# Kernel optimization log

Measured on AMD Instinct MI355X. Metric: run time of the kernel, lower is better.

Reference implementation:

```python
import jax, jax.numpy as jnp
import numpy as np

N = 100000      # nodes
E = 1600000     # edges
G = 1024        # graphs in batch
NF = 9          # atom features (OGB AtomEncoder)
V = 128         # vocab per atom feature
H = 128         # hidden_dim
L = 3           # num_graph_layers
OUT = 10        # output_dim
BN_EPS = 1e-5


def setup_inputs() -> dict:
    key = jax.random.key(0)
    ks = jax.random.split(key, 12)
    x = jax.random.randint(ks[0], (N, NF), 0, V, dtype=jnp.int32)
    edge_index = jax.random.randint(ks[1], (2, E), 0, N, dtype=jnp.int32)
    batch = jnp.sort(jax.random.randint(ks[2], (N,), 0, G, dtype=jnp.int32))
    emb = jax.random.normal(ks[3], (NF, V, H), dtype=jnp.float32) * 0.05
    Ws = jax.random.normal(ks[4], (L, H, H), dtype=jnp.float32) * (1.0 / np.sqrt(H))
    bs = jnp.zeros((L, H), dtype=jnp.float32)
    gamma = jnp.ones((L - 1, H), dtype=jnp.float32)
    beta = jnp.zeros((L - 1, H), dtype=jnp.float32)
    run_mean = jax.random.normal(ks[5], (L - 1, H), dtype=jnp.float32) * 0.1
    run_var = jax.random.uniform(ks[6], (L - 1, H), minval=0.5, maxval=1.5, dtype=jnp.float32)
    W_clf = jax.random.normal(ks[7], (H, OUT), dtype=jnp.float32) * (1.0 / np.sqrt(H))
    b_clf = jnp.zeros((OUT,), dtype=jnp.float32)
    return {"x": x, "edge_index": edge_index, "batch": batch, "emb": emb,
            "Ws": Ws, "bs": bs, "gamma": gamma, "beta": beta,
            "run_mean": run_mean, "run_var": run_var,
            "W_clf": W_clf, "b_clf": b_clf}


def reference(x, edge_index, batch, emb, Ws, bs, gamma, beta, run_mean, run_var, W_clf, b_clf):
    # Eval-mode forward: dropout = identity, BatchNorm uses running stats.
    src, dst = edge_index[0], edge_index[1]
    # GCN symmetric normalization with self-loops: deg = 1 + in-degree
    deg = jax.ops.segment_sum(jnp.ones((E,), jnp.float32), dst, num_segments=N) + 1.0
    dinv = jax.lax.rsqrt(deg)                 # [N]
    norm_e = dinv[src] * dinv[dst]            # [E] edge coefficient
    norm_self = dinv * dinv                   # [N] self-loop coefficient

    # AtomEncoder: sum of per-feature embedding lookups -> [N, H]
    h = emb[jnp.arange(NF)[None, :], x].sum(axis=1)

    for i in range(L):
        hw = h @ Ws[i]                                                       # [N, H]
        h = (jax.ops.segment_sum(hw[src] * norm_e[:, None], dst, num_segments=N)
             + hw * norm_self[:, None] + bs[i])                              # GCNConv
        if i < L - 1:
            h = (h - run_mean[i]) * (gamma[i] * jax.lax.rsqrt(run_var[i] + BN_EPS)) + beta[i]
            h = jax.nn.relu(h)

    # global mean pool over graphs
    counts = jax.ops.segment_sum(jnp.ones((N,), jnp.float32), batch, num_segments=G)
    pooled = jax.ops.segment_sum(h, batch, num_segments=G) / jnp.maximum(counts, 1.0)[:, None]
    return pooled @ W_clf + b_clf             # [G, OUT]
```

## Files before the change

### kernel.cpp

```cpp
#include <hip/hip_runtime.h>
#include <hip/hip_bf16.h>
#include <hip/hip_fp16.h>

#define NN 100000
#define EE 1600000
#define GG 1024
#define NF 9
#define VV 128
#define HH 128
#define LL 3
#define OUTD 10
#define BN_EPS 1e-5f
#define NB_SCAN 98
#define NBUCK 196
#define BCAP 12288
#define CHUNK 4096
#define NB64 1563

typedef __attribute__((ext_vector_type(8))) short short8;
typedef __attribute__((ext_vector_type(8))) _Float16 half8;
typedef __attribute__((ext_vector_type(4))) float f32x4;

__device__ inline unsigned short f2bf(float x) {
    unsigned u = __float_as_uint(x);
    unsigned r = (u + 0x7fffu + ((u >> 16) & 1u)) >> 16;
    return (unsigned short)r;
}
__device__ inline float bf2f(unsigned short b) { return __uint_as_float(((unsigned)b) << 16); }

__device__ inline void mix8(float a[8], const uint4& r, float nm) {
    asm("v_fma_mix_f32 %0, %8, %12, %0 op_sel:[0,0,0] op_sel_hi:[1,0,0]\n\t"
        "v_fma_mix_f32 %1, %8, %12, %1 op_sel:[1,0,0] op_sel_hi:[1,0,0]\n\t"
        "v_fma_mix_f32 %2, %9, %12, %2 op_sel:[0,0,0] op_sel_hi:[1,0,0]\n\t"
        "v_fma_mix_f32 %3, %9, %12, %3 op_sel:[1,0,0] op_sel_hi:[1,0,0]\n\t"
        "v_fma_mix_f32 %4, %10, %12, %4 op_sel:[0,0,0] op_sel_hi:[1,0,0]\n\t"
        "v_fma_mix_f32 %5, %10, %12, %5 op_sel:[1,0,0] op_sel_hi:[1,0,0]\n\t"
        "v_fma_mix_f32 %6, %11, %12, %6 op_sel:[0,0,0] op_sel_hi:[1,0,0]\n\t"
        "v_fma_mix_f32 %7, %11, %12, %7 op_sel:[1,0,0] op_sel_hi:[1,0,0]"
        : "+v"(a[0]), "+v"(a[1]), "+v"(a[2]), "+v"(a[3]),
          "+v"(a[4]), "+v"(a[5]), "+v"(a[6]), "+v"(a[7])
        : "v"(r.x), "v"(r.y), "v"(r.z), "v"(r.w), "v"(nm));
}

__device__ inline void fma4(float4& a, const float4 r, float nm) {
    a.x = fmaf(r.x, nm, a.x); a.y = fmaf(r.y, nm, a.y);
    a.z = fmaf(r.z, nm, a.z); a.w = fmaf(r.w, nm, a.w);
}

__global__ __launch_bounds__(256) void split_kernel(const int* __restrict__ src,
                                                    const int* __restrict__ dst,
                                                    int* __restrict__ bcur,
                                                    int* __restrict__ bucket_edges) {
    __shared__ int lcnt[256], loff[256], lcur[256], gbase[256], sh[256];
    __shared__ int stage[CHUNK];
    __shared__ unsigned char stageb[CHUNK];
    int tid = threadIdx.x;
    int cs = blockIdx.x * CHUNK;
    int n = min(CHUNK, EE - cs);
    lcnt[tid] = 0;
    __syncthreads();
    for (int i = tid; i < n; i += 256)
        atomicAdd(&lcnt[dst[cs + i] >> 9], 1);
    __syncthreads();
    int val = lcnt[tid];
    sh[tid] = val; __syncthreads();
    for (int d = 1; d < 256; d <<= 1) {
        int t = (tid >= d) ? sh[tid - d] : 0;
        __syncthreads();
        sh[tid] += t;
        __syncthreads();
    }
    loff[tid] = sh[tid] - val;
    lcur[tid] = sh[tid] - val;
    __syncthreads();
    for (int i = tid; i < n; i += 256) {
        int d = dst[cs + i], s = src[cs + i];
        int b = d >> 9;
        int p = atomicAdd(&lcur[b], 1);
        stage[p] = (s << 9) | (d & 511);
        stageb[p] = (unsigned char)b;
    }
    if (val > 0) gbase[tid] = atomicAdd(&bcur[tid], val);
    __syncthreads();
    for (int i = tid; i < n; i += 256) {
        int b = stageb[i];
        bucket_edges[(size_t)b * BCAP + gbase[b] + (i - loff[b])] = stage[i];
    }
}

__global__ __launch_bounds__(256) void bhist_kernel(const int* __restrict__ bcur,
                                                    const int* __restrict__ bucket_edges,
                                                    int* __restrict__ cnt) {
    __shared__ int lc[512];
    int b = blockIdx.x, tid = threadIdx.x;
    lc[tid] = 0; lc[tid + 256] = 0;
    __syncthreads();
    int n = bcur[b];
    const int* be = bucket_edges + (size_t)b * BCAP;
    for (int i = tid; i < n; i += 256) atomicAdd(&lc[be[i] & 511], 1);
    __syncthreads();
    int node = b * 512 + tid;
    if (node < NN) cnt[node] = lc[tid];
    node += 256;
    if (node < NN) cnt[node] = lc[tid + 256];
}

__global__ void scanA_kernel(const int* __restrict__ cnt, int* __restrict__ bsum,
                             float* __restrict__ dinv) {
    __shared__ int sh[256];
    int tid = threadIdx.x;
    int base = blockIdx.x * 1024 + tid * 4;
    int s = 0;
#pragma unroll
    for (int i = 0; i < 4; ++i) {
        int idx = base + i;
        if (idx < NN) {
            int c = cnt[idx];
            s += c;
            dinv[idx] = rsqrtf(1.0f + (float)c);
        }
    }
    sh[tid] = s; __syncthreads();
    for (int d = 128; d > 0; d >>= 1) { if (tid < d) sh[tid] += sh[tid + d]; __syncthreads(); }
    if (tid == 0) bsum[blockIdx.x] = sh[0];
}

__global__ void scanB_kernel(int* __restrict__ bsum) {
    __shared__ int sh[128];
    int tid = threadIdx.x;
    int v = (tid < NB_SCAN) ? bsum[tid] : 0;
    sh[tid] = v; __syncthreads();
    for (int d = 1; d < 128; d <<= 1) {
        int t = (tid >= d) ? sh[tid - d] : 0;
        __syncthreads();
        sh[tid] += t;
        __syncthreads();
    }
    if (tid < NB_SCAN) bsum[tid] = sh[tid] - v;
}

__global__ void scanC_kernel(const int* __restrict__ cnt, const int* __restrict__ bsum,
                             int* __restrict__ row_ptr) {
    __shared__ int sh[256];
    int tid = threadIdx.x;
    int base = blockIdx.x * 1024 + tid * 4;
    int v[4];
#pragma unroll
    for (int i = 0; i < 4; ++i) { int idx = base + i; v[i] = (idx < NN) ? cnt[idx] : 0; }
    int tsum = v[0] + v[1] + v[2] + v[3];
    sh[tid] = tsum; __syncthreads();
    for (int d = 1; d < 256; d <<= 1) {
        int t = (tid >= d) ? sh[tid - d] : 0;
        __syncthreads();
        sh[tid] += t;
        __syncthreads();
    }
    int excl = sh[tid] - tsum + bsum[blockIdx.x];
#pragma unroll
    for (int i = 0; i < 4; ++i) {
        int idx = base + i;
        if (idx < NN) row_ptr[idx] = excl;
        excl += v[i];
    }
    if (blockIdx.x == 0 && tid == 0) row_ptr[NN] = EE;
}

__global__ __launch_bounds__(256) void cscatter_kernel(const int* __restrict__ bcur,
                                                       const int* __restrict__ bucket_edges,
                                                       const int* __restrict__ row_ptr,
                                                       const float* __restrict__ dinv,
                                                       int2* __restrict__ col) {
    __shared__ int lcur[512];
    int b = blockIdx.x, tid = threadIdx.x;
    int node0 = b * 512;
#pragma unroll
    for (int k = 0; k < 2; ++k) {
        int j = tid + k * 256;
        int node = node0 + j;
        if (node < NN) lcur[j] = row_ptr[node];
    }
    __syncthreads();
    int n = bcur[b];
    const int* be = bucket_edges + (size_t)b * BCAP;
    for (int i = tid; i < n; i += 256) {
        int w = be[i];
        int j = w & 511;
        int s = (int)((unsigned)w >> 9);
        int p = atomicAdd(&lcur[j], 1);
        float nm = dinv[s] * dinv[node0 + j];
        col[p] = make_int2(s, __float_as_int(nm));
    }
}

__global__ void wconv_kernel(const float* __restrict__ Ws,
                             unsigned short* __restrict__ WThi,
                             unsigned short* __restrict__ WTlo) {
    int id = blockIdx.x * 256 + threadIdx.x;
    if (id >= LL * HH * HH) return;
    int layer = id >> 14;
    int rem = id & (HH * HH - 1);
    int k = rem >> 7, n = rem & 127;
    float w = Ws[id];
    unsigned short hi = f2bf(w);
    float lo = w - bf2f(hi);
    WThi[(size_t)layer * HH * HH + n * HH + k] = hi;
    WTlo[(size_t)layer * HH * HH + n * HH + k] = f2bf(lo);
}

__global__ __launch_bounds__(256) void prep_clf_kernel(const float* __restrict__ Wc,
        const float* __restrict__ b2,
        _Float16* __restrict__ WcThi, _Float16* __restrict__ WcTlo,
        float* __restrict__ bb2) {
    int tid = threadIdx.x;
    for (int id = tid; id < 16 * HH; id += 256) {
        int n = id >> 7, k = id & 127;
        float w = (n < OUTD) ? Wc[k * OUTD + n] : 0.f;
        _Float16 hi = (_Float16)w;
        float lo = w - (float)hi;
        WcThi[id] = hi;
        WcTlo[id] = (_Float16)lo;
    }
    if (tid < OUTD) {
        float s = 0.f;
        for (int c = 0; c < HH; ++c) s += b2[c] * Wc[c * OUTD + tid];
        bb2[tid] = s;
    }
}

__global__ __launch_bounds__(256) void enc_mm_kernel(const int* __restrict__ x,
        const float* __restrict__ emb,
        const unsigned short* __restrict__ WThi, const unsigned short* __restrict__ WTlo,
        __half* __restrict__ hw_out) {
    __shared__ __align__(16) unsigned short lh[32][136];
    __shared__ __align__(16) unsigned short ll[32][136];
    int tid = threadIdx.x;
    int nloc = tid >> 3;
    int seg = tid & 7;
    int nodebase = blockIdx.x * 32;
    int n = nodebase + nloc;
    float s[16];
#pragma unroll
    for (int i = 0; i < 16; ++i) s[i] = 0.f;
#pragma unroll
    for (int f = 0; f < NF; ++f) {
        int idx = x[n * NF + f];
        const float4* ep = (const float4*)(emb + ((size_t)(f * VV + idx)) * HH + seg * 16);
#pragma unroll
        for (int q = 0; q < 4; ++q) {
            float4 e = ep[q];
            s[q * 4 + 0] += e.x; s[q * 4 + 1] += e.y;
            s[q * 4 + 2] += e.z; s[q * 4 + 3] += e.w;
        }
    }
#pragma unroll
    for (int q = 0; q < 4; ++q) {
        ushort4 oh, ol;
        oh.x = f2bf(s[q * 4 + 0]); ol.x = f2bf(s[q * 4 + 0] - bf2f(oh.x));
        oh.y = f2bf(s[q * 4 + 1]); ol.y = f2bf(s[q * 4 + 1] - bf2f(oh.y));
        oh.z = f2bf(s[q * 4 + 2]); ol.z = f2bf(s[q * 4 + 2] - bf2f(oh.z));
        oh.w = f2bf(s[q * 4 + 3]); ol.w = f2bf(s[q * 4 + 3] - bf2f(oh.w));
        *(ushort4*)&lh[nloc][seg * 16 + q * 4] = oh;
        *(ushort4*)&ll[nloc][seg * 16 + q * 4] = ol;
    }
    __syncthreads();
    int wave = tid >> 6, lane = tid & 63;
    int quad = lane >> 4, m = lane & 15;
    f32x4 acc[2][2] = {};
    int kq = quad * 8;
#pragma unroll
    for (int t = 0; t < 4; ++t) {
        int k0 = t * 32 + kq;
        short8 a0h = *(const short8*)&lh[m][k0];
        short8 a0l = *(const short8*)&ll[m][k0];
        short8 a1h = *(const short8*)&lh[16 + m][k0];
        short8 a1l = *(const short8*)&ll[16 + m][k0];
#pragma unroll
        for (int c = 0; c < 2; ++c) {
            int ct = wave * 2 + c;
            short8 bh = *(const short8*)(WThi + (size_t)(ct * 16 + m) * HH + k0);
            short8 bl = *(const short8*)(WTlo + (size_t)(ct * 16 + m) * HH + k0);
            acc[0][c] = __builtin_amdgcn_mfma_f32_16x16x32_bf16(a0h, bh, acc[0][c], 0, 0, 0);
            acc[0][c] = __builtin_amdgcn_mfma_f32_16x16x32_bf16(a0l, bh, acc[0][c], 0, 0, 0);
            acc[0][c] = __builtin_amdgcn_mfma_f32_16x16x32_bf16(a0h, bl, acc[0][c], 0, 0, 0);
            acc[1][c] = __builtin_amdgcn_mfma_f32_16x16x32_bf16(a1h, bh, acc[1][c], 0, 0, 0);
            acc[1][c] = __builtin_amdgcn_mfma_f32_16x16x32_bf16(a1l, bh, acc[1][c], 0, 0, 0);
            acc[1][c] = __builtin_amdgcn_mfma_f32_16x16x32_bf16(a1h, bl, acc[1][c], 0, 0, 0);
        }
    }
#pragma unroll
    for (int c = 0; c < 2; ++c) {
        int colx = (wave * 2 + c) * 16 + m;
#pragma unroll
        for (int rt = 0; rt < 2; ++rt) {
            int r0 = nodebase + rt * 16 + quad * 4;
#pragma unroll
            for (int reg = 0; reg < 4; ++reg)
                hw_out[(size_t)(r0 + reg) * HH + colx] = __float2half(acc[rt][c][reg]);
        }
    }
}

__device__ inline void gather_node(const uint4* __restrict__ hw4,
                                   const int2* __restrict__ col,
                                   int start, int end, int c4,
                                   float a[8], float b[8]) {
    int e = start;
    for (; e + 4 <= end; e += 4) {
        unsigned long long w0 = *(const unsigned long long*)&col[e];
        unsigned long long w1 = *(const unsigned long long*)&col[e + 1];
        unsigned long long w2 = *(const unsigned long long*)&col[e + 2];
        unsigned long long w3 = *(const unsigned long long*)&col[e + 3];
        uint4 r0 = hw4[(size_t)(unsigned)(w0 & 0xffffffffu) * 16 + c4];
        uint4 r1 = hw4[(size_t)(unsigned)(w1 & 0xffffffffu) * 16 + c4];
        uint4 r2 = hw4[(size_t)(unsigned)(w2 & 0xffffffffu) * 16 + c4];
        uint4 r3 = hw4[(size_t)(unsigned)(w3 & 0xffffffffu) * 16 + c4];
        mix8(a, r0, __int_as_float((int)(unsigned)(w0 >> 32)));
        mix8(b, r1, __int_as_float((int)(unsigned)(w1 >> 32)));
        mix8(a, r2, __int_as_float((int)(unsigned)(w2 >> 32)));
        mix8(b, r3, __int_as_float((int)(unsigned)(w3 >> 32)));
    }
    if (e < end) {
        int last = end - 1;
        int e1 = min(e + 1, last), e2 = min(e + 2, last), e3 = min(e + 3, last);
        unsigned long long w0 = *(const unsigned long long*)&col[e];
        unsigned long long w1 = *(const unsigned long long*)&col[e1];
        unsigned long long w2 = *(const unsigned long long*)&col[e2];
        unsigned long long w3 = *(const unsigned long long*)&col[e3];
        float n0 = __int_as_float((int)(unsigned)(w0 >> 32));
        float n1 = (e + 1 < end) ? __int_as_float((int)(unsigned)(w1 >> 32)) : 0.f;
        float n2 = (e + 2 < end) ? __int_as_float((int)(unsigned)(w2 >> 32)) : 0.f;
        float n3 = (e + 3 < end) ? __int_as_float((int)(unsigned)(w3 >> 32)) : 0.f;
        uint4 r0 = hw4[(size_t)(unsigned)(w0 & 0xffffffffu) * 16 + c4];
        uint4 r1 = hw4[(size_t)(unsigned)(w1 & 0xffffffffu) * 16 + c4];
        uint4 r2 = hw4[(size_t)(unsigned)(w2 & 0xffffffffu) * 16 + c4];
        uint4 r3 = hw4[(size_t)(unsigned)(w3 & 0xffffffffu) * 16 + c4];
        mix8(a, r0, n0);
        mix8(b, r1, n1);
        mix8(a, r2, n2);
        mix8(b, r3, n3);
    }
}

__global__ __launch_bounds__(512) void agg_mm_kernel(const __half* __restrict__ hw_in,
    const int* __restrict__ row_ptr, const int2* __restrict__ col,
    const float* __restrict__ dinv,
    const float* __restrict__ bias, const float* __restrict__ gamma,
    const float* __restrict__ beta, const float* __restrict__ rmean,
    const float* __restrict__ rvar,
    const unsigned short* __restrict__ WThi, const unsigned short* __restrict__ WTlo,
    __half* __restrict__ hw_out) {
    __shared__ __align__(16) unsigned short lh[32][136];
    __shared__ __align__(16) unsigned short ll[32][136];
    int wave = threadIdx.x >> 6;
    int lane = threadIdx.x & 63;
    int grp = lane >> 4;
    int c4 = lane & 15;
    int nodebase = blockIdx.x * 32;
    const uint4* hw4 = (const uint4*)hw_in;

    int v = nodebase + wave * 4 + grp;
    int start = row_ptr[v], end = row_ptr[v + 1];
    float a[8] = {}, b[8] = {};
    gather_node(hw4, col, start, end, c4, a, b);

    {
        float dv = dinv[v];
        uint4 r = hw4[(size_t)v * 16 + c4];
        mix8(a, r, dv * dv);
    }
#pragma unroll
    for (int i = 0; i < 8; ++i) a[i] += b[i];

    int ch = c4 * 8;
#pragma unroll
    for (int i = 0; i < 8; ++i) a[i] += bias[ch + i];
#pragma unroll
    for (int i = 0; i < 8; ++i) {
        int c = ch + i;
        float sc = gamma[c] * rsqrtf(rvar[c] + BN_EPS);
        a[i] = fmaxf((a[i] - rmean[c]) * sc + beta[c], 0.f);
    }
    int rloc = wave * 4 + grp;
    ushort4 oh0, oh1, ol0, ol1;
    oh0.x = f2bf(a[0]); ol0.x = f2bf(a[0] - bf2f(oh0.x));
    oh0.y = f2bf(a[1]); ol0.y = f2bf(a[1] - bf2f(oh0.y));
    oh0.z = f2bf(a[2]); ol0.z = f2bf(a[2] - bf2f(oh0.z));
    oh0.w = f2bf(a[3]); ol0.w = f2bf(a[3] - bf2f(oh0.w));
    oh1.x = f2bf(a[4]); ol1.x = f2bf(a[4] - bf2f(oh1.x));
    oh1.y = f2bf(a[5]); ol1.y = f2bf(a[5] - bf2f(oh1.y));
    oh1.z = f2bf(a[6]); ol1.z = f2bf(a[6] - bf2f(oh1.z));
    oh1.w = f2bf(a[7]); ol1.w = f2bf(a[7] - bf2f(oh1.w));
    *(ushort4*)&lh[rloc][ch]     = oh0;
    *(ushort4*)&lh[rloc][ch + 4] = oh1;
    *(ushort4*)&ll[rloc][ch]     = ol0;
    *(ushort4*)&ll[rloc][ch + 4] = ol1;

    __syncthreads();
    int quad = lane >> 4, m = lane & 15;
    f32x4 acc[2] = {};
    int kq = quad * 8;
    int ct = wave;
#pragma unroll
    for (int t = 0; t < 4; ++t) {
        int k0 = t * 32 + kq;
        short8 a0h = *(const short8*)&lh[m][k0];
        short8 a0l = *(const short8*)&ll[m][k0];
        short8 a1h = *(const short8*)&lh[16 + m][k0];
        short8 a1l = *(const short8*)&ll[16 + m][k0];
        short8 bh = *(const short8*)(WThi + (size_t)(ct * 16 + m) * HH + k0);
        short8 bl = *(const short8*)(WTlo + (size_t)(ct * 16 + m) * HH + k0);
        acc[0] = __builtin_amdgcn_mfma_f32_16x16x32_bf16(a0h, bh, acc[0], 0, 0, 0);
        acc[0] = __builtin_amdgcn_mfma_f32_16x16x32_bf16(a0l, bh, acc[0], 0, 0, 0);
        acc[0] = __builtin_amdgcn_mfma_f32_16x16x32_bf16(a0h, bl, acc[0], 0, 0, 0);
        acc[1] = __builtin_amdgcn_mfma_f32_16x16x32_bf16(a1h, bh, acc[1], 0, 0, 0);
        acc[1] = __builtin_amdgcn_mfma_f32_16x16x32_bf16(a1l, bh, acc[1], 0, 0, 0);
        acc[1] = __builtin_amdgcn_mfma_f32_16x16x32_bf16(a1h, bl, acc[1], 0, 0, 0);
    }
    int colx = ct * 16 + m;
#pragma unroll
    for (int rt = 0; rt < 2; ++rt) {
        int r0 = nodebase + rt * 16 + quad * 4;
#pragma unroll
        for (int reg = 0; reg < 4; ++reg)
            hw_out[(size_t)(r0 + reg) * HH + colx] = __float2half(acc[rt][reg]);
    }
}

__global__ __launch_bounds__(256) void yproj_kernel(const __half* __restrict__ hw_in,
        const _Float16* __restrict__ WcThi, const _Float16* __restrict__ WcTlo,
        float* __restrict__ y) {
    int tid = threadIdx.x;
    int wv = tid >> 6, lane = tid & 63;
    int quad = lane >> 4, m = lane & 15;
    int nodebase = blockIdx.x * 64 + wv * 16;
    int an = min(nodebase + m, NN - 1);
    f32x4 acc = {};
#pragma unroll
    for (int t = 0; t < 4; ++t) {
        int k0 = t * 32 + quad * 8;
        half8 a  = *(const half8*)(hw_in + (size_t)an * HH + k0);
        half8 bh = *(const half8*)(WcThi + m * HH + k0);
        half8 bl = *(const half8*)(WcTlo + m * HH + k0);
        acc = __builtin_amdgcn_mfma_f32_16x16x32_f16(a, bh, acc, 0, 0, 0);
        acc = __builtin_amdgcn_mfma_f32_16x16x32_f16(a, bl, acc, 0, 0, 0);
    }
#pragma unroll
    for (int reg = 0; reg < 4; ++reg) {
        int node = nodebase + quad * 4 + reg;
        if (node < NN) y[(size_t)node * 16 + m] = acc[reg];
    }
}

__global__ __launch_bounds__(256) void agg_pool10_kernel(const float* __restrict__ y,
    const int* __restrict__ row_ptr, const int2* __restrict__ col,
    const float* __restrict__ dinv, const int* __restrict__ batch,
    float* __restrict__ pooled) {
    __shared__ __align__(16) float lz[64][16];
    __shared__ int bg[64];
    int tid = threadIdx.x;
    int g4 = tid >> 2;
    int c = tid & 3;
    int nodebase = blockIdx.x * 64;
    int v = nodebase + g4;
    int vc = min(v, NN - 1);
    int start = row_ptr[vc];
    int end = (v < NN) ? row_ptr[vc + 1] : start;
    const float4* y4 = (const float4*)y;
    float4 a = {0.f, 0.f, 0.f, 0.f}, b = {0.f, 0.f, 0.f, 0.f};
    int e = start;
    for (; e + 4 <= end; e += 4) {
        unsigned long long w0 = *(const unsigned long long*)&col[e];
        unsigned long long w1 = *(const unsigned long long*)&col[e + 1];
        unsigned long long w2 = *(const unsigned long long*)&col[e + 2];
        unsigned long long w3 = *(const unsigned long long*)&col[e + 3];
        float4 r0 = y4[(size_t)(unsigned)(w0 & 0xffffffffu) * 4 + c];
        float4 r1 = y4[(size_t)(unsigned)(w1 & 0xffffffffu) * 4 + c];
        float4 r2 = y4[(size_t)(unsigned)(w2 & 0xffffffffu) * 4 + c];
        float4 r3 = y4[(size_t)(unsigned)(w3 & 0xffffffffu) * 4 + c];
        fma4(a, r0, __int_as_float((int)(unsigned)(w0 >> 32)));
        fma4(b, r1, __int_as_float((int)(unsigned)(w1 >> 32)));
        fma4(a, r2, __int_as_float((int)(unsigned)(w2 >> 32)));
        fma4(b, r3, __int_as_float((int)(unsigned)(w3 >> 32)));
    }
    if (e < end) {
        int last = end - 1;
        int e1 = min(e + 1, last), e2 = min(e + 2, last), e3 = min(e + 3, last);
        unsigned long long w0 = *(const unsigned long long*)&col[e];
        unsigned long long w1 = *(const unsigned long long*)&col[e1];
        unsigned long long w2 = *(const unsigned long long*)&col[e2];
        unsigned long long w3 = *(const unsigned long long*)&col[e3];
        float n0 = __int_as_float((int)(unsigned)(w0 >> 32));
        float n1 = (e + 1 < end) ? __int_as_float((int)(unsigned)(w1 >> 32)) : 0.f;
        float n2 = (e + 2 < end) ? __int_as_float((int)(unsigned)(w2 >> 32)) : 0.f;
        float n3 = (e + 3 < end) ? __int_as_float((int)(unsigned)(w3 >> 32)) : 0.f;
        float4 r0 = y4[(size_t)(unsigned)(w0 & 0xffffffffu) * 4 + c];
        float4 r1 = y4[(size_t)(unsigned)(w1 & 0xffffffffu) * 4 + c];
        float4 r2 = y4[(size_t)(unsigned)(w2 & 0xffffffffu) * 4 + c];
        float4 r3 = y4[(size_t)(unsigned)(w3 & 0xffffffffu) * 4 + c];
        fma4(a, r0, n0);
        fma4(b, r1, n1);
        fma4(a, r2, n2);
        fma4(b, r3, n3);
    }
    if (v < NN) {
        float dv = dinv[v];
        float4 r = y4[(size_t)v * 4 + c];
        fma4(a, r, dv * dv);
    }
    a.x += b.x; a.y += b.y; a.z += b.z; a.w += b.w;
    *(float4*)&lz[g4][c * 4] = a;
    if (c == 0) bg[g4] = batch[vc];
    __syncthreads();
    int ch = tid & 15;
    int rh = tid >> 4;
    int r0i = rh * 4;
    int curg = bg[r0i];
    float run = 0.f;
    for (int r = r0i; r < r0i + 4; ++r) {
        int gg = bg[r];
        if (gg != curg) {
            atomicAdd(&pooled[(size_t)curg * 16 + ch], run);
            run = 0.f; curg = gg;
        }
        run += lz[r][ch];
    }
    atomicAdd(&pooled[(size_t)curg * 16 + ch], run);
}

__global__ __launch_bounds__(256) void finalize_kernel(const float* __restrict__ pooled,
    const int* __restrict__ batch, const float* __restrict__ bb2,
    const float* __restrict__ bc, float* __restrict__ out) {
    int id = blockIdx.x * 256 + threadIdx.x;
    if (id >= GG * 16) return;
    int g = id >> 4, o = id & 15;
    if (o >= OUTD) return;
    int lo = 0, hi = NN;
    while (lo < hi) { int mid = (lo + hi) >> 1; if (batch[mid] < g) lo = mid + 1; else hi = mid; }
    int s0 = lo;
    lo = 0; hi = NN;
    int g1 = g + 1;
    while (lo < hi) { int mid = (lo + hi) >> 1; if (batch[mid] < g1) lo = mid + 1; else hi = mid; }
    int cnt = lo - s0;
    float r = pooled[(size_t)g * 16 + o] / fmaxf((float)cnt, 1.0f);
    out[(size_t)g * OUTD + o] = r + ((cnt > 0) ? bb2[o] : 0.f) + bc[o];
}

extern "C" void kernel_launch(void* const* d_in, const int* in_sizes, int n_in,
                              void* d_out, int out_size, void* d_ws, size_t ws_size,
                              hipStream_t stream) {
    const int*   x      = (const int*)d_in[0];
    const int*   eidx   = (const int*)d_in[1];
    const int*   batch  = (const int*)d_in[2];
    const float* emb    = (const float*)d_in[3];
    const float* Ws     = (const float*)d_in[4];
    const float* bs     = (const float*)d_in[5];
    const float* gamma  = (const float*)d_in[6];
    const float* beta   = (const float*)d_in[7];
    const float* rmean  = (const float*)d_in[8];
    const float* rvar   = (const float*)d_in[9];
    const float* Wclf   = (const float*)d_in[10];
    const float* bclf   = (const float*)d_in[11];
    float* out = (float*)d_out;

    const int* e_src = eidx;
    const int* e_dst = eidx + EE;

    char* ws = (char*)d_ws;
    size_t off = 0;
    auto take = [&](size_t bytes) -> void* {
        void* p = ws + off;
        off = (off + bytes + 255) & ~(size_t)255;
        return p;
    };
    float* dinv     = (float*)take((size_t)NN * 4);
    int*   cnt      = (int*)  take((size_t)NN * 4);
    int*   row_ptr  = (int*)  take((size_t)(NN + 1) * 4);
    int*   bsum     = (int*)  take((size_t)NB_SCAN * 4);
    int*   bcur     = (int*)  take((size_t)256 * 4);
    int*   bucket_edges = (int*)take((size_t)NBUCK * BCAP * 4);
    int2*  col      = (int2*) take((size_t)EE * 8);
    __half* hwA     = (__half*)take((size_t)NN * HH * 2);
    __half* hwB     = (__half*)take((size_t)NN * HH * 2);
    float* y        = (float*)take((size_t)NN * 16 * 4);
    float* pooled   = (float*)take((size_t)GG * 16 * 4);
    unsigned short* WThi = (unsigned short*)take((size_t)LL * HH * HH * 2);
    unsigned short* WTlo = (unsigned short*)take((size_t)LL * HH * HH * 2);
    _Float16* WcThi = (_Float16*)take((size_t)16 * HH * 2);
    _Float16* WcTlo = (_Float16*)take((size_t)16 * HH * 2);
    float* bb2      = (float*)take((size_t)16 * 4);

    hipMemsetAsync(bcur, 0, 256 * 4, stream);
    hipMemsetAsync(pooled, 0, (size_t)GG * 16 * 4, stream);

    split_kernel<<<(EE + CHUNK - 1) / CHUNK, 256, 0, stream>>>(e_src, e_dst, bcur, bucket_edges);
    bhist_kernel<<<NBUCK, 256, 0, stream>>>(bcur, bucket_edges, cnt);
    scanA_kernel<<<NB_SCAN, 256, 0, stream>>>(cnt, bsum, dinv);
    scanB_kernel<<<1, 128, 0, stream>>>(bsum);
    scanC_kernel<<<NB_SCAN, 256, 0, stream>>>(cnt, bsum, row_ptr);
    cscatter_kernel<<<NBUCK, 256, 0, stream>>>(bcur, bucket_edges, row_ptr, dinv, col);
    wconv_kernel<<<(LL * HH * HH + 255) / 256, 256, 0, stream>>>(Ws, WThi, WTlo);
    prep_clf_kernel<<<1, 256, 0, stream>>>(Wclf, bs + 2 * HH, WcThi, WcTlo, bb2);

    enc_mm_kernel<<<NN / 32, 256, 0, stream>>>(x, emb, WThi, WTlo, hwA);
    agg_mm_kernel<<<NN / 32, 512, 0, stream>>>(hwA, row_ptr, col, dinv,
        bs, gamma, beta, rmean, rvar,
        WThi + (size_t)1 * HH * HH, WTlo + (size_t)1 * HH * HH, hwB);
    agg_mm_kernel<<<NN / 32, 512, 0, stream>>>(hwB, row_ptr, col, dinv,
        bs + HH, gamma + HH, beta + HH, rmean + HH, rvar + HH,
        WThi + (size_t)2 * HH * HH, WTlo + (size_t)2 * HH * HH, hwA);
    yproj_kernel<<<NB64, 256, 0, stream>>>(hwA, WcThi, WcTlo, y);
    agg_pool10_kernel<<<NB64, 256, 0, stream>>>(y, row_ptr, col, dinv, batch, pooled);
    finalize_kernel<<<(GG * 16 + 255) / 256, 256, 0, stream>>>(pooled, batch, bb2, bclf, out);
}
```

Baseline: 412.0 us.

## Gather two nodes per lane group with software-prefetched edge indices in agg_mm

The aggregation-matmul kernel moves from 512 to 256 threads per block, and each 16-lane group now aggregates two adjacent nodes at once. The gather interleaves the two neighbor lists and prefetches the next four column entries per node while the current row loads are in flight, which raises memory-level parallelism per thread and hides index-load latency. Each wave then computes two output column tiles in the MFMA stage, and the col buffer gets slack for the prefetch overread. The trade-off is half as many resident threads per block, more registers per thread, and load imbalance when paired nodes have different degrees.

```diff
diff --git a/kernel.cpp b/kernel.cpp
--- a/kernel.cpp
+++ b/kernel.cpp
@@ -302,9 +302,7 @@
 
 __device__ inline void gather_node(const uint4* __restrict__ hw4,
                                    const int2* __restrict__ col,
-                                   int start, int end, int c4,
-                                   float a[8], float b[8]) {
-    int e = start;
+                                   int e, int end, int c4, float a[8]) {
     for (; e + 4 <= end; e += 4) {
         unsigned long long w0 = *(const unsigned long long*)&col[e];
         unsigned long long w1 = *(const unsigned long long*)&col[e + 1];
@@ -315,9 +313,9 @@
         uint4 r2 = hw4[(size_t)(unsigned)(w2 & 0xffffffffu) * 16 + c4];
         uint4 r3 = hw4[(size_t)(unsigned)(w3 & 0xffffffffu) * 16 + c4];
         mix8(a, r0, __int_as_float((int)(unsigned)(w0 >> 32)));
-        mix8(b, r1, __int_as_float((int)(unsigned)(w1 >> 32)));
+        mix8(a, r1, __int_as_float((int)(unsigned)(w1 >> 32)));
         mix8(a, r2, __int_as_float((int)(unsigned)(w2 >> 32)));
-        mix8(b, r3, __int_as_float((int)(unsigned)(w3 >> 32)));
+        mix8(a, r3, __int_as_float((int)(unsigned)(w3 >> 32)));
     }
     if (e < end) {
         int last = end - 1;
@@ -335,13 +333,68 @@
         uint4 r2 = hw4[(size_t)(unsigned)(w2 & 0xffffffffu) * 16 + c4];
         uint4 r3 = hw4[(size_t)(unsigned)(w3 & 0xffffffffu) * 16 + c4];
         mix8(a, r0, n0);
-        mix8(b, r1, n1);
+        mix8(a, r1, n1);
         mix8(a, r2, n2);
-        mix8(b, r3, n3);
-    }
-}
-
-__global__ __launch_bounds__(512) void agg_mm_kernel(const __half* __restrict__ hw_in,
+        mix8(a, r3, n3);
+    }
+}
+
+__device__ inline void gather_pair(const uint4* __restrict__ hw4,
+                                   const int2* __restrict__ col,
+                                   int eu, int endu, int ev, int endv, int c4,
+                                   float aU[8], float aV[8]) {
+    if (eu + 4 <= endu && ev + 4 <= endv) {
+        unsigned long long cu0 = *(const unsigned long long*)&col[eu];
+        unsigned long long cu1 = *(const unsigned long long*)&col[eu + 1];
+        unsigned long long cu2 = *(const unsigned long long*)&col[eu + 2];
+        unsigned long long cu3 = *(const unsigned long long*)&col[eu + 3];
+        unsigned long long cv0 = *(const unsigned long long*)&col[ev];
+        unsigned long long cv1 = *(const unsigned long long*)&col[ev + 1];
+        unsigned long long cv2 = *(const unsigned long long*)&col[ev + 2];
+        unsigned long long cv3 = *(const unsigned long long*)&col[ev + 3];
+        while (true) {
+            eu += 4; ev += 4;
+            bool more = (eu + 4 <= endu) && (ev + 4 <= endv);
+            uint4 r0 = hw4[(size_t)(unsigned)(cu0 & 0xffffffffu) * 16 + c4];
+            uint4 r1 = hw4[(size_t)(unsigned)(cu1 & 0xffffffffu) * 16 + c4];
+            uint4 r2 = hw4[(size_t)(unsigned)(cu2 & 0xffffffffu) * 16 + c4];
+            uint4 r3 = hw4[(size_t)(unsigned)(cu3 & 0xffffffffu) * 16 + c4];
+            uint4 s0 = hw4[(size_t)(unsigned)(cv0 & 0xffffffffu) * 16 + c4];
+            uint4 s1 = hw4[(size_t)(unsigned)(cv1 & 0xffffffffu) * 16 + c4];
+            uint4 s2 = hw4[(size_t)(unsigned)(cv2 & 0xffffffffu) * 16 + c4];
+            uint4 s3 = hw4[(size_t)(unsigned)(cv3 & 0xffffffffu) * 16 + c4];
+            float nu0 = __int_as_float((int)(unsigned)(cu0 >> 32));
+            float nu1 = __int_as_float((int)(unsigned)(cu1 >> 32));
+            float nu2 = __int_as_float((int)(unsigned)(cu2 >> 32));
+            float nu3 = __int_as_float((int)(unsigned)(cu3 >> 32));
+            float nv0 = __int_as_float((int)(unsigned)(cv0 >> 32));
+            float nv1 = __int_as_float((int)(unsigned)(cv1 >> 32));
+            float nv2 = __int_as_float((int)(unsigned)(cv2 >> 32));
+            float nv3 = __int_as_float((int)(unsigned)(cv3 >> 32));
+            cu0 = *(const unsigned long long*)&col[eu];
+            cu1 = *(const unsigned long long*)&col[eu + 1];
+            cu2 = *(const unsigned long long*)&col[eu + 2];
+            cu3 = *(const unsigned long long*)&col[eu + 3];
+            cv0 = *(const unsigned long long*)&col[ev];
+            cv1 = *(const unsigned long long*)&col[ev + 1];
+            cv2 = *(const unsigned long long*)&col[ev + 2];
+            cv3 = *(const unsigned long long*)&col[ev + 3];
+            mix8(aU, r0, nu0);
+            mix8(aV, s0, nv0);
+            mix8(aU, r1, nu1);
+            mix8(aV, s1, nv1);
+            mix8(aU, r2, nu2);
+            mix8(aV, s2, nv2);
+            mix8(aU, r3, nu3);
+            mix8(aV, s3, nv3);
+            if (!more) break;
+        }
+    }
+    gather_node(hw4, col, eu, endu, c4, aU);
+    gather_node(hw4, col, ev, endv, c4, aV);
+}
+
+__global__ __launch_bounds__(256) void agg_mm_kernel(const __half* __restrict__ hw_in,
     const int* __restrict__ row_ptr, const int2* __restrict__ col,
     const float* __restrict__ dinv,
     const float* __restrict__ bias, const float* __restrict__ gamma,
@@ -351,55 +404,65 @@
     __half* __restrict__ hw_out) {
     __shared__ __align__(16) unsigned short lh[32][136];
     __shared__ __align__(16) unsigned short ll[32][136];
-    int wave = threadIdx.x >> 6;
-    int lane = threadIdx.x & 63;
+    int tid = threadIdx.x;
+    int wave = tid >> 6;
+    int lane = tid & 63;
     int grp = lane >> 4;
     int c4 = lane & 15;
     int nodebase = blockIdx.x * 32;
     const uint4* hw4 = (const uint4*)hw_in;
 
-    int v = nodebase + wave * 4 + grp;
-    int start = row_ptr[v], end = row_ptr[v + 1];
-    float a[8] = {}, b[8] = {};
-    gather_node(hw4, col, start, end, c4, a, b);
+    int u = nodebase + wave * 8 + grp * 2;
+    int v = u + 1;
+    int su = row_ptr[u];
+    int sv = row_ptr[v];
+    int ev_end = row_ptr[v + 1];
+
+    float aU[8] = {}, aV[8] = {};
+    gather_pair(hw4, col, su, sv, sv, ev_end, c4, aU, aV);
 
     {
+        float du = dinv[u];
+        uint4 r = hw4[(size_t)u * 16 + c4];
+        mix8(aU, r, du * du);
         float dv = dinv[v];
-        uint4 r = hw4[(size_t)v * 16 + c4];
-        mix8(a, r, dv * dv);
-    }
-#pragma unroll
-    for (int i = 0; i < 8; ++i) a[i] += b[i];
+        uint4 q = hw4[(size_t)v * 16 + c4];
+        mix8(aV, q, dv * dv);
+    }
 
     int ch = c4 * 8;
-#pragma unroll
-    for (int i = 0; i < 8; ++i) a[i] += bias[ch + i];
 #pragma unroll
     for (int i = 0; i < 8; ++i) {
         int c = ch + i;
         float sc = gamma[c] * rsqrtf(rvar[c] + BN_EPS);
-        a[i] = fmaxf((a[i] - rmean[c]) * sc + beta[c], 0.f);
-    }
-    int rloc = wave * 4 + grp;
-    ushort4 oh0, oh1, ol0, ol1;
-    oh0.x = f2bf(a[0]); ol0.x = f2bf(a[0] - bf2f(oh0.x));
-    oh0.y = f2bf(a[1]); ol0.y = f2bf(a[1] - bf2f(oh0.y));
-    oh0.z = f2bf(a[2]); ol0.z = f2bf(a[2] - bf2f(oh0.z));
-    oh0.w = f2bf(a[3]); ol0.w = f2bf(a[3] - bf2f(oh0.w));
-    oh1.x = f2bf(a[4]); ol1.x = f2bf(a[4] - bf2f(oh1.x));
-    oh1.y = f2bf(a[5]); ol1.y = f2bf(a[5] - bf2f(oh1.y));
-    oh1.z = f2bf(a[6]); ol1.z = f2bf(a[6] - bf2f(oh1.z));
-    oh1.w = f2bf(a[7]); ol1.w = f2bf(a[7] - bf2f(oh1.w));
-    *(ushort4*)&lh[rloc][ch]     = oh0;
-    *(ushort4*)&lh[rloc][ch + 4] = oh1;
-    *(ushort4*)&ll[rloc][ch]     = ol0;
-    *(ushort4*)&ll[rloc][ch + 4] = ol1;
+        float off = bias[c] - rmean[c];
+        aU[i] = fmaxf((aU[i] + off) * sc + beta[c], 0.f);
+        aV[i] = fmaxf((aV[i] + off) * sc + beta[c], 0.f);
+    }
+    int ru = wave * 8 + grp * 2;
+#pragma unroll
+    for (int half = 0; half < 2; ++half) {
+        const float* a = half ? aV : aU;
+        int r = ru + half;
+        ushort4 oh0, oh1, ol0, ol1;
+        oh0.x = f2bf(a[0]); ol0.x = f2bf(a[0] - bf2f(oh0.x));
+        oh0.y = f2bf(a[1]); ol0.y = f2bf(a[1] - bf2f(oh0.y));
+        oh0.z = f2bf(a[2]); ol0.z = f2bf(a[2] - bf2f(oh0.z));
+        oh0.w = f2bf(a[3]); ol0.w = f2bf(a[3] - bf2f(oh0.w));
+        oh1.x = f2bf(a[4]); ol1.x = f2bf(a[4] - bf2f(oh1.x));
+        oh1.y = f2bf(a[5]); ol1.y = f2bf(a[5] - bf2f(oh1.y));
+        oh1.z = f2bf(a[6]); ol1.z = f2bf(a[6] - bf2f(oh1.z));
+        oh1.w = f2bf(a[7]); ol1.w = f2bf(a[7] - bf2f(oh1.w));
+        *(ushort4*)&lh[r][ch]     = oh0;
+        *(ushort4*)&lh[r][ch + 4] = oh1;
+        *(ushort4*)&ll[r][ch]     = ol0;
+        *(ushort4*)&ll[r][ch + 4] = ol1;
+    }
 
     __syncthreads();
     int quad = lane >> 4, m = lane & 15;
-    f32x4 acc[2] = {};
+    f32x4 acc[2][2] = {};
     int kq = quad * 8;
-    int ct = wave;
 #pragma unroll
     for (int t = 0; t < 4; ++t) {
         int k0 = t * 32 + kq;
@@ -407,22 +470,29 @@
         short8 a0l = *(const short8*)&ll[m][k0];
         short8 a1h = *(const short8*)&lh[16 + m][k0];
         short8 a1l = *(const short8*)&ll[16 + m][k0];
-        short8 bh = *(const short8*)(WThi + (size_t)(ct * 16 + m) * HH + k0);
-        short8 bl = *(const short8*)(WTlo + (size_t)(ct * 16 + m) * HH + k0);
-        acc[0] = __builtin_amdgcn_mfma_f32_16x16x32_bf16(a0h, bh, acc[0], 0, 0, 0);
-        acc[0] = __builtin_amdgcn_mfma_f32_16x16x32_bf16(a0l, bh, acc[0], 0, 0, 0);
-        acc[0] = __builtin_amdgcn_mfma_f32_16x16x32_bf16(a0h, bl, acc[0], 0, 0, 0);
-        acc[1] = __builtin_amdgcn_mfma_f32_16x16x32_bf16(a1h, bh, acc[1], 0, 0, 0);
-        acc[1] = __builtin_amdgcn_mfma_f32_16x16x32_bf16(a1l, bh, acc[1], 0, 0, 0);
-        acc[1] = __builtin_amdgcn_mfma_f32_16x16x32_bf16(a1h, bl, acc[1], 0, 0, 0);
-    }
-    int colx = ct * 16 + m;
-#pragma unroll
-    for (int rt = 0; rt < 2; ++rt) {
-        int r0 = nodebase + rt * 16 + quad * 4;
-#pragma unroll
-        for (int reg = 0; reg < 4; ++reg)
-            hw_out[(size_t)(r0 + reg) * HH + colx] = __float2half(acc[rt][reg]);
+#pragma unroll
+        for (int c = 0; c < 2; ++c) {
+            int ct = wave * 2 + c;
+            short8 bh = *(const short8*)(WThi + (size_t)(ct * 16 + m) * HH + k0);
+            short8 bl = *(const short8*)(WTlo + (size_t)(ct * 16 + m) * HH + k0);
+            acc[0][c] = __builtin_amdgcn_mfma_f32_16x16x32_bf16(a0h, bh, acc[0][c], 0, 0, 0);
+            acc[0][c] = __builtin_amdgcn_mfma_f32_16x16x32_bf16(a0l, bh, acc[0][c], 0, 0, 0);
+            acc[0][c] = __builtin_amdgcn_mfma_f32_16x16x32_bf16(a0h, bl, acc[0][c], 0, 0, 0);
+            acc[1][c] = __builtin_amdgcn_mfma_f32_16x16x32_bf16(a1h, bh, acc[1][c], 0, 0, 0);
+            acc[1][c] = __builtin_amdgcn_mfma_f32_16x16x32_bf16(a1l, bh, acc[1][c], 0, 0, 0);
+            acc[1][c] = __builtin_amdgcn_mfma_f32_16x16x32_bf16(a1h, bl, acc[1][c], 0, 0, 0);
+        }
+    }
+#pragma unroll
+    for (int c = 0; c < 2; ++c) {
+        int colx = (wave * 2 + c) * 16 + m;
+#pragma unroll
+        for (int rt = 0; rt < 2; ++rt) {
+            int r0 = nodebase + rt * 16 + quad * 4;
+#pragma unroll
+            for (int reg = 0; reg < 4; ++reg)
+                hw_out[(size_t)(r0 + reg) * HH + colx] = __float2half(acc[rt][c][reg]);
+        }
     }
 }
 
@@ -578,7 +648,7 @@
     int*   bsum     = (int*)  take((size_t)NB_SCAN * 4);
     int*   bcur     = (int*)  take((size_t)256 * 4);
     int*   bucket_edges = (int*)take((size_t)NBUCK * BCAP * 4);
-    int2*  col      = (int2*) take((size_t)EE * 8);
+    int2*  col      = (int2*) take((size_t)EE * 8 + 64);
     __half* hwA     = (__half*)take((size_t)NN * HH * 2);
     __half* hwB     = (__half*)take((size_t)NN * HH * 2);
     float* y        = (float*)take((size_t)NN * 16 * 4);
@@ -602,10 +672,10 @@
     prep_clf_kernel<<<1, 256, 0, stream>>>(Wclf, bs + 2 * HH, WcThi, WcTlo, bb2);
 
     enc_mm_kernel<<<NN / 32, 256, 0, stream>>>(x, emb, WThi, WTlo, hwA);
-    agg_mm_kernel<<<NN / 32, 512, 0, stream>>>(hwA, row_ptr, col, dinv,
+    agg_mm_kernel<<<NN / 32, 256, 0, stream>>>(hwA, row_ptr, col, dinv,
         bs, gamma, beta, rmean, rvar,
         WThi + (size_t)1 * HH * HH, WTlo + (size_t)1 * HH * HH, hwB);
-    agg_mm_kernel<<<NN / 32, 512, 0, stream>>>(hwB, row_ptr, col, dinv,
+    agg_mm_kernel<<<NN / 32, 256, 0, stream>>>(hwB, row_ptr, col, dinv,
         bs + HH, gamma + HH, beta + HH, rmean + HH, rvar + HH,
         WThi + (size_t)2 * HH * HH, WTlo + (size_t)2 * HH * HH, hwA);
     yproj_kernel<<<NB64, 256, 0, stream>>>(hwA, WcThi, WcTlo, y);
```

After: 428.3 us. 1.04x slower.
